# Kernel tuning notes

Hardware: AMD Instinct MI355X
Metric: run time of the kernel (lower is better)

The kernel has to match this reference:

```python
import jax, jax.numpy as jnp
import numpy as np

B, S, D = 2, 2048, 2048
H, KVH, HD = 16, 4, 128
REP = H // KVH  # 4
THETA = 10000.0


def setup_inputs() -> dict:
    key = jax.random.key(0)
    ks = jax.random.split(key, 5)
    scale = 0.02
    x = jax.random.normal(ks[0], (B, S, D), dtype=jnp.float32)
    Wq = jax.random.normal(ks[1], (D, H * HD), dtype=jnp.float32) * scale
    Wk = jax.random.normal(ks[2], (D, KVH * HD), dtype=jnp.float32) * scale
    Wv = jax.random.normal(ks[3], (D, KVH * HD), dtype=jnp.float32) * scale
    Wo = jax.random.normal(ks[4], (H * HD, D), dtype=jnp.float32) * scale
    return {"x": x, "Wq": Wq, "Wk": Wk, "Wv": Wv, "Wo": Wo}


def _rope_cos_sin(seq_len, dtype):
    # HF-style rotary embedding: inv_freq over even dims, duplicated halves
    inv_freq = 1.0 / (THETA ** (jnp.arange(0, HD, 2, dtype=jnp.float32) / HD))
    pos = jnp.arange(seq_len, dtype=jnp.float32)
    ang = pos[:, None] * inv_freq[None, :]          # [S, HD/2]
    emb = jnp.concatenate([ang, ang], axis=-1)       # [S, HD]
    return jnp.cos(emb).astype(dtype), jnp.sin(emb).astype(dtype)


def _rotate_half(t):
    t1, t2 = jnp.split(t, 2, axis=-1)
    return jnp.concatenate([-t2, t1], axis=-1)


def reference(x, Wq, Wk, Wv, Wo):
    bsz, seq_len, _ = x.shape
    q = (x @ Wq).reshape(bsz, seq_len, H, HD).transpose(0, 2, 1, 3)    # [B,H,S,HD]
    k = (x @ Wk).reshape(bsz, seq_len, KVH, HD).transpose(0, 2, 1, 3)  # [B,KVH,S,HD]
    v = (x @ Wv).reshape(bsz, seq_len, KVH, HD).transpose(0, 2, 1, 3)
    cos, sin = _rope_cos_sin(seq_len, q.dtype)       # [S,HD]
    cos = cos[None, None, :, :]
    sin = sin[None, None, :, :]
    q = q * cos + _rotate_half(q) * sin
    k = k * cos + _rotate_half(k) * sin
    # repeat_interleave KV heads to match Q heads
    k = jnp.repeat(k, REP, axis=1)                   # [B,H,S,HD]
    v = jnp.repeat(v, REP, axis=1)
    scores = jnp.einsum('bhqd,bhkd->bhqk', q, k) / jnp.sqrt(jnp.float32(HD)).astype(q.dtype)
    i = jnp.arange(seq_len)
    causal = jnp.where(i[None, :] > i[:, None], jnp.float32(-jnp.inf), 0.0).astype(scores.dtype)
    scores = scores + causal[None, None, :, :]
    probs = jax.nn.softmax(scores.astype(jnp.float32), axis=-1).astype(q.dtype)
    out = jnp.einsum('bhqk,bhkd->bhqd', probs, v)    # [B,H,S,HD]
    out = out.transpose(0, 2, 1, 3).reshape(bsz, seq_len, H * HD)
    return out @ Wo
```

## Files before the change

### kernel.cpp

```cpp
#include <hip/hip_runtime.h>
#include <math.h>

#define B_   2
#define S_   2048
#define D_   2048
#define H_   16
#define KVH_ 4
#define HD_  128
#define REP_ 4

typedef __attribute__((ext_vector_type(8))) short bf16x8;
typedef __attribute__((ext_vector_type(4))) short bf16x4;
typedef __attribute__((ext_vector_type(4))) float f32x4;

#define QSCALE_LOG2E 0.1275266977097153f

__device__ __forceinline__ unsigned short f2bf(float x) {
    union { float f; unsigned u; } v; v.f = x;
    unsigned r = v.u + 0x7FFF + ((v.u >> 16) & 1);
    return (unsigned short)(r >> 16);
}

__device__ __forceinline__ unsigned short f2bf_fast(float x) {
    union { float f; unsigned u; } v; v.f = x;
    return (unsigned short)((v.u + 0x8000) >> 16);
}

__device__ __forceinline__ void gl_lds16(const unsigned short* g, unsigned short* l) {
    __builtin_amdgcn_global_load_lds(
        (const __attribute__((address_space(1))) unsigned int*)g,
        (__attribute__((address_space(3))) unsigned int*)l,
        16, 0, 0);
}

#define PH_BAR() do { asm volatile("" ::: "memory"); \
                      __builtin_amdgcn_s_barrier();  \
                      asm volatile("" ::: "memory"); } while (0)
#define VMW6 asm volatile("s_waitcnt vmcnt(6)" ::: "memory")
#define VMW0 asm volatile("s_waitcnt vmcnt(0)" ::: "memory")

__global__ void cast_bf16(const float* __restrict__ src,
                          unsigned short* __restrict__ dst, int n4)
{
    int i = blockIdx.x * 256 + threadIdx.x;
    if (i >= n4) return;
    float4 v = *(const float4*)&src[(size_t)i * 4];
    bf16x4 o;
    o[0] = (short)f2bf(v.x); o[1] = (short)f2bf(v.y);
    o[2] = (short)f2bf(v.z); o[3] = (short)f2bf(v.w);
    *(bf16x4*)&dst[(size_t)i * 4] = o;
}

__global__ __launch_bounds__(256) void cast_transpose_all(
    const float* __restrict__ Wq, const float* __restrict__ Wk,
    const float* __restrict__ Wv, const float* __restrict__ Wo,
    unsigned short* __restrict__ Wqt, unsigned short* __restrict__ Wkt,
    unsigned short* __restrict__ Wvt, unsigned short* __restrict__ Wot)
{
    __shared__ float T[32][33];
    const int y = blockIdx.y;
    const float* src; unsigned short* dst; int C, bj;
    if (y < 64)      { src = Wq; dst = Wqt; C = 2048; bj = y; }
    else if (y < 80) { src = Wk; dst = Wkt; C = 512;  bj = y - 64; }
    else if (y < 96) { src = Wv; dst = Wvt; C = 512;  bj = y - 80; }
    else             { src = Wo; dst = Wot; C = 2048; bj = y - 96; }

    const int bi = blockIdx.x;
    const int t  = threadIdx.x;
    const int r  = t >> 3, cq = (t & 7) * 4;

    float4 v = *(const float4*)&src[(size_t)(bi * 32 + r) * C + bj * 32 + cq];
    T[r][cq + 0] = v.x; T[r][cq + 1] = v.y;
    T[r][cq + 2] = v.z; T[r][cq + 3] = v.w;
    __syncthreads();

    bf16x4 o;
    o[0] = (short)f2bf(T[cq + 0][r]);
    o[1] = (short)f2bf(T[cq + 1][r]);
    o[2] = (short)f2bf(T[cq + 2][r]);
    o[3] = (short)f2bf(T[cq + 3][r]);
    *(bf16x4*)&dst[(size_t)(bj * 32 + r) * 2048 + bi * 32 + cq] = o;
}

__global__ __launch_bounds__(512, 2) void qkv_mfma8(
    const unsigned short* __restrict__ Ah,
    const unsigned short* __restrict__ Wqt,
    const unsigned short* __restrict__ Wkt,
    const unsigned short* __restrict__ Wvt,
    unsigned short* __restrict__ Qh, unsigned short* __restrict__ Kh,
    unsigned short* __restrict__ Vt)
{
    __shared__ __align__(16) unsigned short lds[65536];

    const int bid = blockIdx.x;
    const int swz = (bid & 7) * 24 + (bid >> 3);
    const int bm = swz / 12, bn = swz % 12;
    const int m0 = bm * 256, n0 = bn * 256;

    const int tid  = threadIdx.x;
    const int w    = tid >> 6;
    const int lane = tid & 63;
    const int lo16 = lane & 15, quad = lane >> 4;
    const int wm   = w >> 2, wn = w & 3;

    const unsigned short* Bt;
    if (n0 < 2048)      Bt = Wqt + (size_t)n0 * 2048;
    else if (n0 < 2560) Bt = Wkt + (size_t)(n0 - 2048) * 2048;
    else                Bt = Wvt + (size_t)(n0 - 2560) * 2048;
    const unsigned short* Ag   = Ah + (size_t)m0 * 2048;
    const unsigned short* AgH1 = Ag + (size_t)128 * 2048;
    const unsigned short* BtH1 = Bt + (size_t)128 * 2048;

    const int rs   = lane >> 3;
    const int sce  = (((lane & 7) ^ rs) << 3);
    const int grow = w * 8 + rs;

    #define STAGE(gb, k0, lb) do {                                          \
        const unsigned short* _g = (gb) + (size_t)grow * 2048 + (k0) + sce; \
        gl_lds16(_g,                     (lb) + w * 512);                   \
        gl_lds16(_g + (size_t)64 * 2048, (lb) + (8 + w) * 512);             \
    } while (0)

    const int swb = (lo16 & 7) << 4;
    const int ac0 = (quad << 4) ^ swb;
    const int ac1 = (64 | (quad << 4)) ^ swb;
    char* ldsb = (char*)lds;
    const int abase = (wm * 128 + lo16) * 128;
    const int bbase = (wn * 16 + lo16) * 128 + 32768;

    f32x4 acc[8][4];
    #pragma unroll
    for (int mf = 0; mf < 8; ++mf)
        #pragma unroll
        for (int j = 0; j < 4; ++j) acc[mf][j] = (f32x4){0.f, 0.f, 0.f, 0.f};

    bf16x8 a0[4][2], a1[4][2], b0[2][2], b1[2][2];

    #define MM(Aa, Bb, mo, jo)                                               \
        _Pragma("unroll") for (int mf = 0; mf < 4; ++mf)                     \
        _Pragma("unroll") for (int j = 0; j < 2; ++j) {                      \
            acc[(mo)+mf][(jo)+j] = __builtin_amdgcn_mfma_f32_16x16x32_bf16(  \
                Aa[mf][0], Bb[j][0], acc[(mo)+mf][(jo)+j], 0, 0, 0);         \
            acc[(mo)+mf][(jo)+j] = __builtin_amdgcn_mfma_f32_16x16x32_bf16(  \
                Aa[mf][1], Bb[j][1], acc[(mo)+mf][(jo)+j], 0, 0, 0);         \
        }

    STAGE(Bt,   0,  lds + 16384);
    STAGE(BtH1, 0,  lds + 24576);
    STAGE(Ag,   0,  lds + 0);
    STAGE(AgH1, 0,  lds + 8192);
    STAGE(Bt,   64, lds + 32768 + 16384);
    STAGE(BtH1, 64, lds + 32768 + 24576);
    STAGE(Ag,   64, lds + 32768);
    VMW6;
    PH_BAR();

    #define PHASES(p, t)                                                         \
    {                              \
        _Pragma("unroll") for (int mf = 0; mf < 4; ++mf) {                       \
            a0[mf][0] = *(const bf16x8*)(ldsb + (p)*65536 + abase + mf*2048 + ac0); \
            a0[mf][1] = *(const bf16x8*)(ldsb + (p)*65536 + abase + mf*2048 + ac1); \
        }                                                                        \
        _Pragma("unroll") for (int j = 0; j < 2; ++j) {                          \
            b0[j][0] = *(const bf16x8*)(ldsb + (p)*65536 + bbase + j*8192 + ac0); \
            b0[j][1] = *(const bf16x8*)(ldsb + (p)*65536 + bbase + j*8192 + ac1); \
        }                                                                        \
        STAGE(AgH1, ((t)+1)*64, lds + ((p)^1)*32768 + 8192);                     \
        PH_BAR(); __builtin_amdgcn_s_setprio(1);                                 \
        MM(a0, b0, 0, 0);                                                        \
        __builtin_amdgcn_s_setprio(0); PH_BAR();                                 \
                                             \
        _Pragma("unroll") for (int j = 0; j < 2; ++j) {                          \
            b1[j][0] = *(const bf16x8*)(ldsb + (p)*65536 + bbase + (j+2)*8192 + ac0); \
            b1[j][1] = *(const bf16x8*)(ldsb + (p)*65536 + bbase + (j+2)*8192 + ac1); \
        }                                                                        \
        STAGE(Bt, ((t)+2)*64, lds + (p)*32768 + 16384);                          \
        PH_BAR(); __builtin_amdgcn_s_setprio(1);                                 \
        MM(a0, b1, 0, 2);                                                        \
        __builtin_amdgcn_s_setprio(0); PH_BAR();                                 \
                                             \
        _Pragma("unroll") for (int mf = 0; mf < 4; ++mf) {                       \
            a1[mf][0] = *(const bf16x8*)(ldsb + (p)*65536 + abase + (mf+4)*2048 + ac0); \
            a1[mf][1] = *(const bf16x8*)(ldsb + (p)*65536 + abase + (mf+4)*2048 + ac1); \
        }                                                                        \
        STAGE(BtH1, ((t)+2)*64, lds + (p)*32768 + 24576);                        \
        PH_BAR(); __builtin_amdgcn_s_setprio(1);                                 \
        MM(a1, b0, 4, 0);                                                        \
        __builtin_amdgcn_s_setprio(0); PH_BAR();                                 \
                                  \
        STAGE(Ag, ((t)+2)*64, lds + (p)*32768);                                  \
        PH_BAR(); __builtin_amdgcn_s_setprio(1);                                 \
        MM(a1, b1, 4, 2);                                                        \
        __builtin_amdgcn_s_setprio(0);                                           \
        VMW6;                                                                    \
        PH_BAR();                                                                \
    }

    for (int it = 0; it < 16; ++it) {
        const int t = 2 * it;
        PHASES(0, t);
        PHASES(1, t + 1);
    }

    VMW0;
    PH_BAR();

    const int bb = m0 >> 11;
    const int s0loc = m0 & 2047;

    if (n0 < 2560) {
        const bool isQ = (n0 < 2048);
        const int h0 = isQ ? (n0 >> 7) : ((n0 - 2048) >> 7);
        const float post = isQ ? QSCALE_LOG2E : 1.0f;
        unsigned short* db[2];
        #pragma unroll
        for (int hp = 0; hp < 2; ++hp)
            db[hp] = isQ
                ? Qh + (((size_t)bb * H_   + h0 + hp) * S_) * HD_
                : Kh + (((size_t)bb * KVH_ + h0 + hp) * S_) * HD_;
        const int d = wn * 16 + lo16;
        const float inv = exp2f(-(float)d * 0.20761871093344086f);
        #pragma unroll
        for (int mf = 0; mf < 8; ++mf) {
            #pragma unroll
            for (int r = 0; r < 4; ++r) {
                int s = s0loc + wm * 128 + mf * 16 + quad * 4 + r;
                float sn, c;
                sincosf((float)s * inv, &sn, &c);
                #pragma unroll
                for (int hp = 0; hp < 2; ++hp) {
                    float lo = acc[mf][2 * hp + 0][r];
                    float hi = acc[mf][2 * hp + 1][r];
                    unsigned short* drow = db[hp] + (size_t)s * HD_;
                    drow[d]      = f2bf((lo * c - hi * sn) * post);
                    drow[d + 64] = f2bf((hi * c + lo * sn) * post);
                }
            }
        }
    } else {
        const int g0 = (n0 - 2560) >> 7;
        unsigned short* Ts = lds;
        const int d = wn * 16 + lo16;
        #pragma unroll
        for (int hp = 0; hp < 2; ++hp) {
            if (hp) PH_BAR();
            #pragma unroll
            for (int mf = 0; mf < 8; ++mf) {
                int ml = wm * 128 + mf * 16 + quad * 4;
                bf16x4 v0, v1;
                #pragma unroll
                for (int r = 0; r < 4; ++r) {
                    v0[r] = (short)f2bf(acc[mf][2 * hp + 0][r]);
                    v1[r] = (short)f2bf(acc[mf][2 * hp + 1][r]);
                }
                *(bf16x4*)&Ts[(size_t)d        * 264 + ml] = v0;
                *(bf16x4*)&Ts[(size_t)(d + 64) * 264 + ml] = v1;
            }
            PH_BAR();
            unsigned short* dstb = Vt + (((size_t)bb * KVH_ + g0 + hp) * HD_) * S_ + s0loc;
            #pragma unroll
            for (int itb = 0; itb < 8; ++itb) {
                int dd = itb * 16 + (tid >> 5);
                int ch = (tid & 31) * 8;
                *(bf16x8*)(dstb + (size_t)dd * S_ + ch) =
                    *(const bf16x8*)&Ts[(size_t)dd * 264 + ch];
            }
        }
    }
    #undef PHASES
    #undef MM
    #undef STAGE
}

__global__ __launch_bounds__(256, 2) void flash_attn_mfma(
    const unsigned short* __restrict__ Qh,
    const unsigned short* __restrict__ Kh,
    const unsigned short* __restrict__ Vt,
    unsigned short* __restrict__ attb)
{
    const int bh   = blockIdx.x;
    const int yy   = blockIdx.y;
    const int qt   = (yy < 8) ? (15 - yy) : (yy - 8);
    const int b    = bh >> 4, h = bh & 15;
    const int g    = h >> 2;
    const int tid  = threadIdx.x;
    const int w    = tid >> 6;
    const int lane = tid & 63;
    const int lo16 = lane & 15;
    const int quad = lane >> 4;

    const unsigned short* Qb = Qh + (((size_t)b * H_   + h) * S_) * HD_;
    const unsigned short* Kb = Kh + (((size_t)b * KVH_ + g) * S_) * HD_;
    const unsigned short* Vb = Vt + (((size_t)b * KVH_ + g) * HD_) * S_;

    __shared__ __align__(16) unsigned short Ks[64][136];
    __shared__ __align__(16) unsigned short Vs[128][72];
    __shared__ __align__(16) unsigned short Ps[4][32][72];

    const int q0 = qt * 128;
    const int qw = q0 + w * 32;

    bf16x8 qf[2][4];
    #pragma unroll
    for (int st = 0; st < 2; ++st)
        #pragma unroll
        for (int kc = 0; kc < 4; ++kc)
            qf[st][kc] = *(const bf16x8*)(Qb + (size_t)(qw + st * 16 + lo16) * HD_
                                             + kc * 32 + quad * 8);

    f32x4 o[2][8];
    #pragma unroll
    for (int st = 0; st < 2; ++st)
        #pragma unroll
        for (int n = 0; n < 8; ++n) o[st][n] = (f32x4){0.f, 0.f, 0.f, 0.f};
    float l_loc[2][4];
    #pragma unroll
    for (int st = 0; st < 2; ++st)
        #pragma unroll
        for (int r = 0; r < 4; ++r) l_loc[st][r] = 0.0f;

    const int kr = tid >> 4, kch = (tid & 15) * 8;
    const int vr = tid >> 3, vch = (tid & 7) * 8;

    bf16x8 kreg[4], vreg[4];
    #pragma unroll
    for (int i = 0; i < 4; ++i) {
        kreg[i] = *(const bf16x8*)(Kb + (size_t)(16 * i + kr) * HD_ + kch);
        vreg[i] = *(const bf16x8*)(Vb + (size_t)(32 * i + vr) * S_ + vch);
    }

    const int ktend = 2 * qt + 1;
    for (int kt = 0; kt <= ktend; ++kt) {
        const int k0 = kt * 64;
        __syncthreads();
        #pragma unroll
        for (int i = 0; i < 4; ++i) {
            *(bf16x8*)&Ks[16 * i + kr][kch] = kreg[i];
            *(bf16x8*)&Vs[32 * i + vr][vch] = vreg[i];
        }
        if (kt < ktend) {
            const int k0n = k0 + 64;
            #pragma unroll
            for (int i = 0; i < 4; ++i) {
                kreg[i] = *(const bf16x8*)(Kb + (size_t)(k0n + 16 * i + kr) * HD_ + kch);
                vreg[i] = *(const bf16x8*)(Vb + (size_t)(32 * i + vr) * S_ + k0n + vch);
            }
        }
        __syncthreads();

        if (w >= 2 || kt < ktend) {
            f32x4 sc[2][4];
            #pragma unroll
            for (int st = 0; st < 2; ++st)
                #pragma unroll
                for (int cb = 0; cb < 4; ++cb) sc[st][cb] = (f32x4){0.f, 0.f, 0.f, 0.f};
            #pragma unroll
            for (int kc = 0; kc < 4; ++kc)
                #pragma unroll
                for (int cb = 0; cb < 4; ++cb) {
                    bf16x8 kf = *(const bf16x8*)&Ks[cb * 16 + lo16][kc * 32 + quad * 8];
                    #pragma unroll
                    for (int st = 0; st < 2; ++st)
                        sc[st][cb] = __builtin_amdgcn_mfma_f32_16x16x32_bf16(
                            qf[st][kc], kf, sc[st][cb], 0, 0, 0);
                }

            const bool masked = (w < 2) ? (kt == 2 * qt) : (kt == ktend);
            if (masked) {
                #pragma unroll
                for (int st = 0; st < 2; ++st)
                    #pragma unroll
                    for (int r = 0; r < 4; ++r) {
                        const int row = qw + st * 16 + quad * 4 + r;
                        float lacc = 0.0f;
                        #pragma unroll
                        for (int cb = 0; cb < 4; ++cb) {
                            float xv = sc[st][cb][r];
                            if ((k0 + cb * 16 + lo16) > row) xv = -1e30f;
                            float p = exp2f(xv);
                            lacc += p;
                            Ps[w][st * 16 + quad * 4 + r][cb * 16 + lo16] = f2bf_fast(p);
                        }
                        l_loc[st][r] += lacc;
                    }
            } else {
                #pragma unroll
                for (int st = 0; st < 2; ++st)
                    #pragma unroll
                    for (int r = 0; r < 4; ++r) {
                        float lacc = 0.0f;
                        #pragma unroll
                        for (int cb = 0; cb < 4; ++cb) {
                            float p = exp2f(sc[st][cb][r]);
                            lacc += p;
                            Ps[w][st * 16 + quad * 4 + r][cb * 16 + lo16] = f2bf_fast(p);
                        }
                        l_loc[st][r] += lacc;
                    }
            }

            #pragma unroll
            for (int kc = 0; kc < 2; ++kc) {
                bf16x8 pf[2];
                #pragma unroll
                for (int st = 0; st < 2; ++st)
                    pf[st] = *(const bf16x8*)&Ps[w][st * 16 + lo16][kc * 32 + quad * 8];
                #pragma unroll
                for (int n = 0; n < 8; ++n) {
                    bf16x8 vf = *(const bf16x8*)&Vs[n * 16 + lo16][kc * 32 + quad * 8];
                    #pragma unroll
                    for (int st = 0; st < 2; ++st)
                        o[st][n] = __builtin_amdgcn_mfma_f32_16x16x32_bf16(
                            pf[st], vf, o[st][n], 0, 0, 0);
                }
            }
        }
    }

    #pragma unroll
    for (int st = 0; st < 2; ++st)
        #pragma unroll
        for (int r = 0; r < 4; ++r) {
            float l = l_loc[st][r];
            l += __shfl_xor(l, 1);
            l += __shfl_xor(l, 2);
            l += __shfl_xor(l, 4);
            l += __shfl_xor(l, 8);
            float invl = 1.0f / l;
            int srow = qw + st * 16 + quad * 4 + r;
            unsigned short* dst = attb + ((size_t)b * S_ + srow) * D_ + h * HD_;
            #pragma unroll
            for (int n = 0; n < 8; ++n)
                dst[n * 16 + lo16] = f2bf(o[st][n][r] * invl);
        }
}

__global__ __launch_bounds__(256) void out_mfma(
    const unsigned short* __restrict__ Ah,
    const unsigned short* __restrict__ Wot,
    float* __restrict__ C)
{
    __shared__ __align__(16) unsigned short As[128 * 32];
    __shared__ __align__(16) unsigned short Bs[128 * 32];

    const int bm = blockIdx.x, bn = blockIdx.y;
    const int m0 = bm * 128, n0 = bn * 128;
    const int tid  = threadIdx.x;
    const int w    = tid >> 6;
    const int lane = tid & 63;
    const int lo16 = lane & 15, quad = lane >> 4;
    const int wm   = w >> 1, wn = w & 1;
    const int cmap[4] = { wn * 2, wn * 2 + 1, wn * 2 + 4, wn * 2 + 5 };

    const unsigned short* Ag = Ah  + (size_t)m0 * 2048;
    const unsigned short* Bt = Wot + (size_t)n0 * 2048;

    f32x4 acc[4][4];
    #pragma unroll
    for (int im = 0; im < 4; ++im)
        #pragma unroll
        for (int jn = 0; jn < 4; ++jn) acc[im][jn] = (f32x4){0.f, 0.f, 0.f, 0.f};

    const int srow = w * 32 + (lane >> 2);
    const int scol = (lane & 3) * 8;

    for (int kt = 0; kt < 2048; kt += 32) {
        __syncthreads();
        gl_lds16(Ag + (size_t)(srow     ) * 2048 + kt + scol, As + (w * 32     ) * 32);
        gl_lds16(Ag + (size_t)(srow + 16) * 2048 + kt + scol, As + (w * 32 + 16) * 32);
        gl_lds16(Bt + (size_t)(srow     ) * 2048 + kt + scol, Bs + (w * 32     ) * 32);
        gl_lds16(Bt + (size_t)(srow + 16) * 2048 + kt + scol, Bs + (w * 32 + 16) * 32);
        __syncthreads();

        bf16x8 af[4], bf[4];
        #pragma unroll
        for (int im = 0; im < 4; ++im)
            af[im] = *(const bf16x8*)&As[(wm * 64 + im * 16 + lo16) * 32 + quad * 8];
        #pragma unroll
        for (int jn = 0; jn < 4; ++jn)
            bf[jn] = *(const bf16x8*)&Bs[(cmap[jn] * 16 + lo16) * 32 + quad * 8];
        #pragma unroll
        for (int im = 0; im < 4; ++im)
            #pragma unroll
            for (int jn = 0; jn < 4; ++jn)
                acc[im][jn] = __builtin_amdgcn_mfma_f32_16x16x32_bf16(
                    af[im], bf[jn], acc[im][jn], 0, 0, 0);
    }

    #pragma unroll
    for (int im = 0; im < 4; ++im)
        #pragma unroll
        for (int r = 0; r < 4; ++r) {
            size_t m = (size_t)(m0 + wm * 64 + im * 16 + quad * 4 + r);
            #pragma unroll
            for (int jn = 0; jn < 4; ++jn)
                C[m * 2048 + n0 + cmap[jn] * 16 + lo16] = acc[im][jn][r];
        }
}

extern "C" void kernel_launch(void* const* d_in, const int* in_sizes, int n_in,
                              void* d_out, int out_size, void* d_ws, size_t ws_size,
                              hipStream_t stream)
{
    const float* x  = (const float*)d_in[0];
    const float* Wq = (const float*)d_in[1];
    const float* Wk = (const float*)d_in[2];
    const float* Wv = (const float*)d_in[3];
    const float* Wo = (const float*)d_in[4];
    float* out = (float*)d_out;

    unsigned short* xh  = (unsigned short*)d_ws;
    unsigned short* Wqt = xh  + (size_t)4096 * 2048;
    unsigned short* Wkt = Wqt + (size_t)2048 * 2048;
    unsigned short* Wvt = Wkt + (size_t)512 * 2048;
    unsigned short* Wot = Wvt + (size_t)512 * 2048;
    unsigned short* Qh  = Wot + (size_t)2048 * 2048;
    unsigned short* Kh  = Qh  + (size_t)B_ * H_   * S_ * HD_;
    unsigned short* Vt  = Kh  + (size_t)B_ * KVH_ * S_ * HD_;
    unsigned short* attb= xh;

    cast_bf16<<<(4096 * 2048 / 4 + 255) / 256, 256, 0, stream>>>(x, xh, 4096 * 2048 / 4);
    cast_transpose_all<<<dim3(64, 160), 256, 0, stream>>>(Wq, Wk, Wv, Wo, Wqt, Wkt, Wvt, Wot);

    qkv_mfma8<<<192, 512, 0, stream>>>(xh, Wqt, Wkt, Wvt, Qh, Kh, Vt);

    flash_attn_mfma<<<dim3(32, 16), 256, 0, stream>>>(Qh, Kh, Vt, attb);

    out_mfma<<<dim3(32, 16), 256, 0, stream>>>(attb, Wot, out);
}
```

Baseline: 293.6 us.

## Rewrite output projection GEMM as 8-wave pipelined kernel with swizzled LDS

Result: faster. 279.6 us (-4.8%).

```diff
diff --git a/kernel.cpp b/kernel.cpp
--- a/kernel.cpp
+++ b/kernel.cpp
@@ -37,6 +37,7 @@
                       __builtin_amdgcn_s_barrier();  \
                       asm volatile("" ::: "memory"); } while (0)
 #define VMW6 asm volatile("s_waitcnt vmcnt(6)" ::: "memory")
+#define VMW4 asm volatile("s_waitcnt vmcnt(4)" ::: "memory")
 #define VMW0 asm volatile("s_waitcnt vmcnt(0)" ::: "memory")
 
 __global__ void cast_bf16(const float* __restrict__ src,
@@ -156,8 +157,7 @@
     PH_BAR();
 
     #define PHASES(p, t)                                                         \
-    {                              \
-        _Pragma("unroll") for (int mf = 0; mf < 4; ++mf) {                       \
+    {   _Pragma("unroll") for (int mf = 0; mf < 4; ++mf) {                       \
             a0[mf][0] = *(const bf16x8*)(ldsb + (p)*65536 + abase + mf*2048 + ac0); \
             a0[mf][1] = *(const bf16x8*)(ldsb + (p)*65536 + abase + mf*2048 + ac1); \
         }                                                                        \
@@ -169,7 +169,6 @@
         PH_BAR(); __builtin_amdgcn_s_setprio(1);                                 \
         MM(a0, b0, 0, 0);                                                        \
         __builtin_amdgcn_s_setprio(0); PH_BAR();                                 \
-                                             \
         _Pragma("unroll") for (int j = 0; j < 2; ++j) {                          \
             b1[j][0] = *(const bf16x8*)(ldsb + (p)*65536 + bbase + (j+2)*8192 + ac0); \
             b1[j][1] = *(const bf16x8*)(ldsb + (p)*65536 + bbase + (j+2)*8192 + ac1); \
@@ -178,7 +177,6 @@
         PH_BAR(); __builtin_amdgcn_s_setprio(1);                                 \
         MM(a0, b1, 0, 2);                                                        \
         __builtin_amdgcn_s_setprio(0); PH_BAR();                                 \
-                                             \
         _Pragma("unroll") for (int mf = 0; mf < 4; ++mf) {                       \
             a1[mf][0] = *(const bf16x8*)(ldsb + (p)*65536 + abase + (mf+4)*2048 + ac0); \
             a1[mf][1] = *(const bf16x8*)(ldsb + (p)*65536 + abase + (mf+4)*2048 + ac1); \
@@ -187,7 +185,6 @@
         PH_BAR(); __builtin_amdgcn_s_setprio(1);                                 \
         MM(a1, b0, 4, 0);                                                        \
         __builtin_amdgcn_s_setprio(0); PH_BAR();                                 \
-                                  \
         STAGE(Ag, ((t)+2)*64, lds + (p)*32768);                                  \
         PH_BAR(); __builtin_amdgcn_s_setprio(1);                                 \
         MM(a1, b1, 4, 2);                                                        \
@@ -435,67 +432,125 @@
         }
 }
 
-__global__ __launch_bounds__(256) void out_mfma(
+__global__ __launch_bounds__(512, 2) void out_mfma8(
     const unsigned short* __restrict__ Ah,
     const unsigned short* __restrict__ Wot,
     float* __restrict__ C)
 {
-    __shared__ __align__(16) unsigned short As[128 * 32];
-    __shared__ __align__(16) unsigned short Bs[128 * 32];
-
-    const int bm = blockIdx.x, bn = blockIdx.y;
-    const int m0 = bm * 128, n0 = bn * 128;
+    __shared__ __align__(16) unsigned short lds[49152];
+
+    const int bid = blockIdx.x;
+    const int swz = (bid & 7) * 32 + (bid >> 3);
+    const int bm = swz >> 4, bn = swz & 15;
+    const int m0 = bm * 256, n0 = bn * 128;
+
     const int tid  = threadIdx.x;
     const int w    = tid >> 6;
     const int lane = tid & 63;
     const int lo16 = lane & 15, quad = lane >> 4;
-    const int wm   = w >> 1, wn = w & 1;
-    const int cmap[4] = { wn * 2, wn * 2 + 1, wn * 2 + 4, wn * 2 + 5 };
-
-    const unsigned short* Ag = Ah  + (size_t)m0 * 2048;
-    const unsigned short* Bt = Wot + (size_t)n0 * 2048;
-
-    f32x4 acc[4][4];
-    #pragma unroll
-    for (int im = 0; im < 4; ++im)
-        #pragma unroll
-        for (int jn = 0; jn < 4; ++jn) acc[im][jn] = (f32x4){0.f, 0.f, 0.f, 0.f};
-
-    const int srow = w * 32 + (lane >> 2);
-    const int scol = (lane & 3) * 8;
-
-    for (int kt = 0; kt < 2048; kt += 32) {
-        __syncthreads();
-        gl_lds16(Ag + (size_t)(srow     ) * 2048 + kt + scol, As + (w * 32     ) * 32);
-        gl_lds16(Ag + (size_t)(srow + 16) * 2048 + kt + scol, As + (w * 32 + 16) * 32);
-        gl_lds16(Bt + (size_t)(srow     ) * 2048 + kt + scol, Bs + (w * 32     ) * 32);
-        gl_lds16(Bt + (size_t)(srow + 16) * 2048 + kt + scol, Bs + (w * 32 + 16) * 32);
-        __syncthreads();
-
-        bf16x8 af[4], bf[4];
-        #pragma unroll
-        for (int im = 0; im < 4; ++im)
-            af[im] = *(const bf16x8*)&As[(wm * 64 + im * 16 + lo16) * 32 + quad * 8];
-        #pragma unroll
-        for (int jn = 0; jn < 4; ++jn)
-            bf[jn] = *(const bf16x8*)&Bs[(cmap[jn] * 16 + lo16) * 32 + quad * 8];
-        #pragma unroll
-        for (int im = 0; im < 4; ++im)
-            #pragma unroll
-            for (int jn = 0; jn < 4; ++jn)
-                acc[im][jn] = __builtin_amdgcn_mfma_f32_16x16x32_bf16(
-                    af[im], bf[jn], acc[im][jn], 0, 0, 0);
-    }
-
-    #pragma unroll
-    for (int im = 0; im < 4; ++im)
+    const int wm   = w >> 2, wn = w & 3;
+
+    const unsigned short* Ag   = Ah  + (size_t)m0 * 2048;
+    const unsigned short* AgH1 = Ag  + (size_t)128 * 2048;
+    const unsigned short* Bt   = Wot + (size_t)n0 * 2048;
+
+    const int rs   = lane >> 3;
+    const int sce  = (((lane & 7) ^ rs) << 3);
+    const int grow = w * 8 + rs;
+
+    #define OSTAGE(gb, k0, lb) do {                                         \
+        const unsigned short* _g = (gb) + (size_t)grow * 2048 + (k0) + sce; \
+        gl_lds16(_g,                     (lb) + w * 512);                   \
+        gl_lds16(_g + (size_t)64 * 2048, (lb) + (8 + w) * 512);             \
+    } while (0)
+
+    const int swb = (lo16 & 7) << 4;
+    const int ac0 = (quad << 4) ^ swb;
+    const int ac1 = (64 | (quad << 4)) ^ swb;
+    char* ldsb = (char*)lds;
+    const int abase = (wm * 128 + lo16) * 128;
+    const int bbase = (wn * 32 + lo16) * 128 + 32768;
+
+    f32x4 acc[8][2];
+    #pragma unroll
+    for (int mf = 0; mf < 8; ++mf)
+        #pragma unroll
+        for (int j = 0; j < 2; ++j) acc[mf][j] = (f32x4){0.f, 0.f, 0.f, 0.f};
+
+    bf16x8 a0[4][2], a1[4][2], bb[2][2];
+
+    #define OMM(Aa, mo, j)                                                   \
+        _Pragma("unroll") for (int mf = 0; mf < 4; ++mf) {                   \
+            acc[(mo)+mf][j] = __builtin_amdgcn_mfma_f32_16x16x32_bf16(       \
+                Aa[mf][0], bb[j][0], acc[(mo)+mf][j], 0, 0, 0);              \
+            acc[(mo)+mf][j] = __builtin_amdgcn_mfma_f32_16x16x32_bf16(       \
+                Aa[mf][1], bb[j][1], acc[(mo)+mf][j], 0, 0, 0);              \
+        }
+
+    OSTAGE(Bt,   0,  lds + 16384);
+    OSTAGE(Ag,   0,  lds + 0);
+    OSTAGE(AgH1, 0,  lds + 8192);
+    OSTAGE(Bt,   64, lds + 24576 + 16384);
+    OSTAGE(Ag,   64, lds + 24576);
+    VMW4;
+    PH_BAR();
+
+    #define OPH(p, t)                                                            \
+    {             \
+        _Pragma("unroll") for (int mf = 0; mf < 4; ++mf) {                       \
+            a0[mf][0] = *(const bf16x8*)(ldsb + (p)*49152 + abase + mf*2048 + ac0); \
+            a0[mf][1] = *(const bf16x8*)(ldsb + (p)*49152 + abase + mf*2048 + ac1); \
+        }                                                                        \
+        _Pragma("unroll") for (int j = 0; j < 2; ++j) {                          \
+            bb[j][0] = *(const bf16x8*)(ldsb + (p)*49152 + bbase + j*2048 + ac0); \
+            bb[j][1] = *(const bf16x8*)(ldsb + (p)*49152 + bbase + j*2048 + ac1); \
+        }                                                                        \
+        OSTAGE(AgH1, ((t)+1)*64, lds + ((p)^1)*24576 + 8192);                    \
+        PH_BAR(); __builtin_amdgcn_s_setprio(1);                                 \
+        OMM(a0, 0, 0);                                                           \
+        __builtin_amdgcn_s_setprio(0); PH_BAR();                                 \
+                                        \
+        OSTAGE(Bt, ((t)+2)*64, lds + (p)*24576 + 16384);                         \
+        PH_BAR(); __builtin_amdgcn_s_setprio(1);                                 \
+        OMM(a0, 0, 1);                                                           \
+        __builtin_amdgcn_s_setprio(0); PH_BAR();                                 \
+                                                \
+        _Pragma("unroll") for (int mf = 0; mf < 4; ++mf) {                       \
+            a1[mf][0] = *(const bf16x8*)(ldsb + (p)*49152 + abase + (mf+4)*2048 + ac0); \
+            a1[mf][1] = *(const bf16x8*)(ldsb + (p)*49152 + abase + (mf+4)*2048 + ac1); \
+        }                                                                        \
+        PH_BAR(); __builtin_amdgcn_s_setprio(1);                                 \
+        OMM(a1, 4, 0);                                                           \
+        __builtin_amdgcn_s_setprio(0); PH_BAR();                                 \
+              \
+        OSTAGE(Ag, ((t)+2)*64, lds + (p)*24576);                                 \
+        PH_BAR(); __builtin_amdgcn_s_setprio(1);                                 \
+        OMM(a1, 4, 1);                                                           \
+        __builtin_amdgcn_s_setprio(0);                                           \
+        VMW4;                                                                    \
+        PH_BAR();                                                                \
+    }
+
+    for (int it = 0; it < 16; ++it) {
+        const int t = 2 * it;
+        OPH(0, t);
+        OPH(1, t + 1);
+    }
+
+    VMW0;
+
+    #pragma unroll
+    for (int mf = 0; mf < 8; ++mf)
         #pragma unroll
         for (int r = 0; r < 4; ++r) {
-            size_t m = (size_t)(m0 + wm * 64 + im * 16 + quad * 4 + r);
-            #pragma unroll
-            for (int jn = 0; jn < 4; ++jn)
-                C[m * 2048 + n0 + cmap[jn] * 16 + lo16] = acc[im][jn][r];
-        }
+            size_t m = (size_t)(m0 + wm * 128 + mf * 16 + quad * 4 + r);
+            #pragma unroll
+            for (int j = 0; j < 2; ++j)
+                C[m * 2048 + n0 + wn * 32 + j * 16 + lo16] = acc[mf][j][r];
+        }
+    #undef OPH
+    #undef OMM
+    #undef OSTAGE
 }
 
 extern "C" void kernel_launch(void* const* d_in, const int* in_sizes, int n_in,
@@ -526,5 +581,5 @@
 
     flash_attn_mfma<<<dim3(32, 16), 256, 0, stream>>>(Qh, Kh, Vt, attb);
 
-    out_mfma<<<dim3(32, 16), 256, 0, stream>>>(attb, Wot, out);
-}
+    out_mfma8<<<256, 512, 0, stream>>>(attb, Wot, out);
+}
```
